# Optimization experiments

Measured on AMD Instinct MI355X. Metric: run time of the kernel, lower is better.

## Reference

```python
import jax, jax.numpy as jnp
import numpy as np


def setup_inputs() -> dict:
    key = jax.random.key(0)
    kx, kwl, kbl, kwr = jax.random.split(key, 4)
    B = 64          # batch of identical DAGs
    L = 11          # number of levels (leaves = level 0)
    NPL = 10000     # nodes per level
    K = 16          # children per non-leaf node
    N = L * NPL     # 110000 nodes per graph
    # Build a layered DAG: edges go child (level l-1) -> father (level l),
    # matching the module's convention edge_index[0]=child, edge_index[1]=father
    # (leaves are nodes with in-degree 0).
    rng = np.random.default_rng(0)
    srcs, dsts = [], []
    for l in range(1, L):
        fathers = np.arange(l * NPL, (l + 1) * NPL)
        children = rng.integers((l - 1) * NPL, l * NPL, size=(NPL, K))
        srcs.append(children.reshape(-1))
        dsts.append(np.repeat(fathers, K))
    edge_index = jnp.asarray(
        np.stack([np.concatenate(srcs), np.concatenate(dsts)]), dtype=jnp.int32
    )  # [2, E] with E = (L-1)*NPL*K = 1.6M
    x = jax.random.normal(kx, (B, N, 1), dtype=jnp.float32)
    w_l = jax.random.normal(kwl, (1, 1), dtype=jnp.float32)   # lin_l weight (1->1)
    b_l = jax.random.normal(kbl, (1,), dtype=jnp.float32) * 0.1  # lin_l bias
    w_r = jax.random.normal(kwr, (1, 1), dtype=jnp.float32)   # lin_r weight (no bias)
    return {"x": x, "w_l": w_l, "b_l": b_l, "w_r": w_r,
            "edge_index": edge_index, "num_levels": L - 1}


def _dagprop(x, w_l, b_l, w_r, edge_index, num_levels):
    # x: [B, N, 1] scalar node features for B identical DAGs.
    src, dst = edge_index[0], edge_index[1]
    N = x.shape[1]
    xb = x[..., 0]  # [B, N]
    indeg = jnp.zeros((N,), jnp.int32).at[dst].add(1)  # in-degree (children count)
    is_leaf = indeg == 0
    # Init: out[leaves] = tanh(x[leaves]); out[non-leaves] = lin_r(x) (no bias).
    out = jnp.where(is_leaf[None, :], jnp.tanh(xb), xb * w_r[0, 0])  # [B, N]
    visited = is_leaf
    inv_deg = 1.0 / jnp.maximum(indeg, 1).astype(xb.dtype)
    for _ in range(num_levels):
        # fathers whose children are ALL visited become the next frontier
        nvis = jnp.zeros((N,), jnp.int32).at[dst].add(visited[src].astype(jnp.int32))
        ready = (~visited) & (indeg > 0) & (nvis == indeg)
        # scatter-mean of children's outputs over all incoming edges (aggr='mean');
        # only consumed at 'ready' nodes, whose children are all visited.
        agg = jnp.zeros_like(out).at[:, dst].add(out[:, src]) * inv_deg[None, :]
        # out[next] = tanh(out[next] + lin_l(agg[next]))
        new = jnp.tanh(out + agg * w_l[0, 0] + b_l[0])
        out = jnp.where(ready[None, :], new, out)
        visited = visited | ready
    return out[..., None]  # [B, N, 1]


def reference(x, w_l, b_l, w_r, edge_index, num_levels):
    return _dagprop(x, w_l, b_l, w_r, edge_index, num_levels)
```

## Files before the change

### kernel.cpp

```cpp
#include <hip/hip_runtime.h>
#include <math.h>

#define BATCH  64
#define NPL    10000
#define NLEV   10
#define NNODE  110000
#define KCH    16
#define GSPLIT 8
#define FPB    (NPL / GSPLIT)
#define NPAIR  (BATCH / 2)
#define THREADS 1024
#define ITER    2

#define EXPITCH_F4 3072
#define EXPITCH_F  (EXPITCH_F4 * 4)
#define EXCH_FLOATS (2 * BATCH * EXPITCH_F)
#define FLAG_STRIDE 128

__device__ inline void coh_store(float* p, float v) {
    __hip_atomic_store(p, v, __ATOMIC_RELAXED, __HIP_MEMORY_SCOPE_AGENT);
}
__device__ inline void flag_set(unsigned char* p) {
    __hip_atomic_store(p, (unsigned char)1, __ATOMIC_RELAXED,
                       __HIP_MEMORY_SCOPE_AGENT);
}
__device__ inline unsigned long long flag_poll(const unsigned long long* p) {
    return __hip_atomic_load(p, __ATOMIC_RELAXED, __HIP_MEMORY_SCOPE_AGENT);
}

__device__ inline void coh_load4_x6(const float4* p0, const float4* p1,
                                    const float4* p2, const float4* p3,
                                    const float4* p4, const float4* p5,
                                    float4& a, float4& b, float4& c,
                                    float4& d, float4& e, float4& f) {
    asm volatile("global_load_dwordx4 %0, %6, off sc0 sc1\n\t"
                 "global_load_dwordx4 %1, %7, off sc0 sc1\n\t"
                 "global_load_dwordx4 %2, %8, off sc0 sc1\n\t"
                 "global_load_dwordx4 %3, %9, off sc0 sc1\n\t"
                 "global_load_dwordx4 %4, %10, off sc0 sc1\n\t"
                 "global_load_dwordx4 %5, %11, off sc0 sc1\n\t"
                 "s_waitcnt vmcnt(0)"
                 : "=&v"(a), "=&v"(b), "=&v"(c), "=&v"(d), "=&v"(e), "=&v"(f)
                 : "v"(p0), "v"(p1), "v"(p2), "v"(p3), "v"(p4), "v"(p5)
                 : "memory");
}

__global__ __launch_bounds__(THREADS, 4) void k_dag_pair(
    const float* __restrict__ x,
    float*       __restrict__ out,
    const int4*  __restrict__ src4,
    float*       __restrict__ exch,
    unsigned char* __restrict__ flags,
    const float* __restrict__ wl_p,
    const float* __restrict__ bl_p,
    const float* __restrict__ wr_p)
{
    __shared__ float bufA[EXPITCH_F];
    __shared__ float bufB[EXPITCH_F];
    const int blk  = blockIdx.x;
    const int pair = blk >> 3;
    const int q    = blk & 7;
    const int gA   = pair * 2, gB = gA + 1;
    const int tid  = threadIdx.x;
    const float wr   = wr_p[0];
    const float wl16 = wl_p[0] * (1.0f / 16.0f);
    const float bl   = bl_p[0];
    const float* __restrict__ xA = x   + (size_t)gA * NNODE;
    const float* __restrict__ xB = x   + (size_t)gB * NNODE;
    float*       __restrict__ oA = out + (size_t)gA * NNODE;
    float*       __restrict__ oB = out + (size_t)gB * NNODE;
    const int f0 = q * FPB;
    unsigned long long* flA = (unsigned long long*)(flags + gA * FLAG_STRIDE);
    unsigned long long* flB = (unsigned long long*)(flags + gB * FLAG_STRIDE);
    const unsigned long long ALL = 0x0101010101010101ULL;

    {
        float* exA0 = exch + (size_t)gA * EXPITCH_F;
        float* exB0 = exch + (size_t)gB * EXPITCH_F;
        for (int i = f0 + tid; i < f0 + FPB; i += THREADS) {
            float vA = tanhf(xA[i]); oA[i] = vA; coh_store(exA0 + i, vA);
            float vB = tanhf(xB[i]); oB[i] = vB; coh_store(exB0 + i, vB);
        }
    }
    __syncthreads();
    if (tid == 0) {
        flag_set((unsigned char*)flA + 0 * 8 + q);
        flag_set((unsigned char*)flB + 0 * 8 + q);
    }

    for (int l = 1; l <= NLEV; ++l) {
        const int pprev = (l - 1) & 1;
        if (tid == 0)
            while (flag_poll(flA + (l - 1)) != ALL) __builtin_amdgcn_s_sleep(1);
        if (tid == 256)
            while (flag_poll(flB + (l - 1)) != ALL) __builtin_amdgcn_s_sleep(1);
        asm volatile("" ::: "memory");
        __syncthreads();

        {
            const float4* eA = (const float4*)(exch +
                ((size_t)pprev * BATCH + gA) * EXPITCH_F);
            const float4* eB = (const float4*)(exch +
                ((size_t)pprev * BATCH + gB) * EXPITCH_F);
            float4 a0, a1, a2, b0, b1, b2;
            coh_load4_x6(eA + tid, eA + tid + 1024, eA + tid + 2048,
                         eB + tid, eB + tid + 1024, eB + tid + 2048,
                         a0, a1, a2, b0, b1, b2);
            float4* vA = (float4*)bufA;  float4* vB = (float4*)bufB;
            vA[tid] = a0; vA[tid + 1024] = a1; vA[tid + 2048] = a2;
            vB[tid] = b0; vB[tid + 1024] = b1; vB[tid + 2048] = b2;
        }
        __syncthreads();

        const int off   = (l - 1) * NPL;
        const int nodeb = l * NPL + f0;
        float* ewA = exch + ((size_t)(l & 1) * BATCH + gA) * EXPITCH_F + f0;
        float* ewB = exch + ((size_t)(l & 1) * BATCH + gB) * EXPITCH_F + f0;
        const int4* sp = src4 + (size_t)((l - 1) * NPL + f0) * (KCH / 4);
#pragma unroll
        for (int it = 0; it < ITER; ++it) {
            const int f = tid + it * THREADS;
            if (f < FPB) {
                const int4 c0 = sp[f * 4 + 0];
                const int4 c1 = sp[f * 4 + 1];
                const int4 c2 = sp[f * 4 + 2];
                const int4 c3 = sp[f * 4 + 3];
                float sA = bufA[c0.x - off] + bufA[c0.y - off]
                         + bufA[c0.z - off] + bufA[c0.w - off]
                         + bufA[c1.x - off] + bufA[c1.y - off]
                         + bufA[c1.z - off] + bufA[c1.w - off]
                         + bufA[c2.x - off] + bufA[c2.y - off]
                         + bufA[c2.z - off] + bufA[c2.w - off]
                         + bufA[c3.x - off] + bufA[c3.y - off]
                         + bufA[c3.z - off] + bufA[c3.w - off];
                float sB = bufB[c0.x - off] + bufB[c0.y - off]
                         + bufB[c0.z - off] + bufB[c0.w - off]
                         + bufB[c1.x - off] + bufB[c1.y - off]
                         + bufB[c1.z - off] + bufB[c1.w - off]
                         + bufB[c2.x - off] + bufB[c2.y - off]
                         + bufB[c2.z - off] + bufB[c2.w - off]
                         + bufB[c3.x - off] + bufB[c3.y - off]
                         + bufB[c3.z - off] + bufB[c3.w - off];
                const float vA = tanhf(fmaf(sA, wl16, fmaf(xA[nodeb + f], wr, bl)));
                const float vB = tanhf(fmaf(sB, wl16, fmaf(xB[nodeb + f], wr, bl)));
                oA[nodeb + f] = vA;
                oB[nodeb + f] = vB;
                if (l < NLEV) { coh_store(ewA + f, vA); coh_store(ewB + f, vB); }
            }
        }
        if (l < NLEV) {
            __syncthreads();
            if (tid == 0) {
                flag_set((unsigned char*)flA + l * 8 + q);
                flag_set((unsigned char*)flB + l * 8 + q);
            }
        }
    }
}

extern "C" void kernel_launch(void* const* d_in, const int* in_sizes, int n_in,
                              void* d_out, int out_size, void* d_ws, size_t ws_size,
                              hipStream_t stream) {
    const float* x  = (const float*)d_in[0];
    const float* wl = (const float*)d_in[1];
    const float* bl = (const float*)d_in[2];
    const float* wr = (const float*)d_in[3];
    const int*   ei = (const int*)d_in[4];

    const int4* src4 = (const int4*)ei;
    float* out  = (float*)d_out;
    float* exch = (float*)d_ws;
    unsigned char* flags = (unsigned char*)d_ws + (size_t)EXCH_FLOATS * sizeof(float);

    hipMemsetAsync(flags, 0, BATCH * FLAG_STRIDE, stream);
    k_dag_pair<<<NPAIR * GSPLIT, THREADS, 0, stream>>>(
        x, out, src4, exch, flags, wl, bl, wr);
}
```

Before: 153.6 us.

## Pipeline per-level exchange loads and publish graph A before graph B

Child indices and x values for each level are now prefetched before spinning on the readiness flags, so their latency hides behind the wait. The exchange loads for both graphs are issued together, but only graph A's data is awaited first. Graph A's gather and tanh run while graph B's loads are still in flight, and A's level flag is published before B is processed, so dependent blocks can start earlier. In exchange, every thread now polls the flags instead of one thread per graph, and correctness depends on hand-placed waitcnt and barrier ordering for the coherent stores.

```diff
diff --git a/kernel.cpp b/kernel.cpp
--- a/kernel.cpp
+++ b/kernel.cpp
@@ -10,7 +10,6 @@
 #define FPB    (NPL / GSPLIT)
 #define NPAIR  (BATCH / 2)
 #define THREADS 1024
-#define ITER    2
 
 #define EXPITCH_F4 3072
 #define EXPITCH_F  (EXPITCH_F4 * 4)
@@ -28,24 +27,41 @@
     return __hip_atomic_load(p, __ATOMIC_RELAXED, __HIP_MEMORY_SCOPE_AGENT);
 }
 
-__device__ inline void coh_load4_x6(const float4* p0, const float4* p1,
-                                    const float4* p2, const float4* p3,
-                                    const float4* p4, const float4* p5,
-                                    float4& a, float4& b, float4& c,
-                                    float4& d, float4& e, float4& f) {
-    asm volatile("global_load_dwordx4 %0, %6, off sc0 sc1\n\t"
-                 "global_load_dwordx4 %1, %7, off sc0 sc1\n\t"
-                 "global_load_dwordx4 %2, %8, off sc0 sc1\n\t"
-                 "global_load_dwordx4 %3, %9, off sc0 sc1\n\t"
-                 "global_load_dwordx4 %4, %10, off sc0 sc1\n\t"
-                 "global_load_dwordx4 %5, %11, off sc0 sc1\n\t"
-                 "s_waitcnt vmcnt(0)"
-                 : "=&v"(a), "=&v"(b), "=&v"(c), "=&v"(d), "=&v"(e), "=&v"(f)
-                 : "v"(p0), "v"(p1), "v"(p2), "v"(p3), "v"(p4), "v"(p5)
-                 : "memory");
+__device__ inline void coh_issue6_waitA(
+    const float4* pa0, const float4* pa1, const float4* pa2,
+    const float4* pb0, const float4* pb1, const float4* pb2,
+    float4& a0, float4& a1, float4& a2,
+    float4& b0, float4& b1, float4& b2) {
+    asm volatile(
+        "global_load_dwordx4 %0, %6, off sc0 sc1\n\t"
+        "global_load_dwordx4 %1, %7, off sc0 sc1\n\t"
+        "global_load_dwordx4 %2, %8, off sc0 sc1\n\t"
+        "global_load_dwordx4 %3, %9, off sc0 sc1\n\t"
+        "global_load_dwordx4 %4, %10, off sc0 sc1\n\t"
+        "global_load_dwordx4 %5, %11, off sc0 sc1\n\t"
+        "s_waitcnt vmcnt(3)"
+        : "=&v"(a0), "=&v"(a1), "=&v"(a2), "=&v"(b0), "=&v"(b1), "=&v"(b2)
+        : "v"(pa0), "v"(pa1), "v"(pa2), "v"(pb0), "v"(pb1), "v"(pb2)
+        : "memory");
+}
+__device__ inline void vm_wait0() {
+    asm volatile("s_waitcnt vmcnt(0)" ::: "memory");
+    __builtin_amdgcn_sched_barrier(0);
+}
+__device__ inline void barrier_lds() {
+    asm volatile("s_waitcnt lgkmcnt(0)" ::: "memory");
+    __builtin_amdgcn_sched_barrier(0);
+    __builtin_amdgcn_s_barrier();
+    __builtin_amdgcn_sched_barrier(0);
 }
 
-__global__ __launch_bounds__(THREADS, 4) void k_dag_pair(
+#define GATHER16(BUF, c0, c1, c2, c3, off)                                  \
+    (BUF[c0.x - off] + BUF[c0.y - off] + BUF[c0.z - off] + BUF[c0.w - off]  \
+   + BUF[c1.x - off] + BUF[c1.y - off] + BUF[c1.z - off] + BUF[c1.w - off]  \
+   + BUF[c2.x - off] + BUF[c2.y - off] + BUF[c2.z - off] + BUF[c2.w - off]  \
+   + BUF[c3.x - off] + BUF[c3.y - off] + BUF[c3.z - off] + BUF[c3.w - off])
+
+__global__ __launch_bounds__(THREADS, 4) void k_dag_pipe(
     const float* __restrict__ x,
     float*       __restrict__ out,
     const int4*  __restrict__ src4,
@@ -84,77 +100,75 @@
     }
     __syncthreads();
     if (tid == 0) {
-        flag_set((unsigned char*)flA + 0 * 8 + q);
-        flag_set((unsigned char*)flB + 0 * 8 + q);
+        flag_set((unsigned char*)flA + q);
+        flag_set((unsigned char*)flB + q);
     }
 
     for (int l = 1; l <= NLEV; ++l) {
         const int pprev = (l - 1) & 1;
-        if (tid == 0)
-            while (flag_poll(flA + (l - 1)) != ALL) __builtin_amdgcn_s_sleep(1);
-        if (tid == 256)
-            while (flag_poll(flB + (l - 1)) != ALL) __builtin_amdgcn_s_sleep(1);
+        const int off   = (l - 1) * NPL;
+        const int nodeb = l * NPL + f0;
+
+        const int4* sp = src4 + (size_t)((l - 1) * NPL + f0) * (KCH / 4);
+        const int4 p0 = sp[tid * 4 + 0];
+        const int4 p1 = sp[tid * 4 + 1];
+        const int4 p2 = sp[tid * 4 + 2];
+        const int4 p3 = sp[tid * 4 + 3];
+        const float xaf = xA[nodeb + tid];
+        const float xbf = xB[nodeb + tid];
+
+        while (flag_poll(flA + (l - 1)) != ALL) __builtin_amdgcn_s_sleep(1);
+        while (flag_poll(flB + (l - 1)) != ALL) __builtin_amdgcn_s_sleep(1);
         asm volatile("" ::: "memory");
-        __syncthreads();
 
-        {
-            const float4* eA = (const float4*)(exch +
-                ((size_t)pprev * BATCH + gA) * EXPITCH_F);
-            const float4* eB = (const float4*)(exch +
-                ((size_t)pprev * BATCH + gB) * EXPITCH_F);
-            float4 a0, a1, a2, b0, b1, b2;
-            coh_load4_x6(eA + tid, eA + tid + 1024, eA + tid + 2048,
+        const float4* eA = (const float4*)(exch + ((size_t)pprev * BATCH + gA) * EXPITCH_F);
+        const float4* eB = (const float4*)(exch + ((size_t)pprev * BATCH + gB) * EXPITCH_F);
+        float4 a0, a1, a2, b0, b1, b2;
+        coh_issue6_waitA(eA + tid, eA + tid + 1024, eA + tid + 2048,
                          eB + tid, eB + tid + 1024, eB + tid + 2048,
                          a0, a1, a2, b0, b1, b2);
-            float4* vA = (float4*)bufA;  float4* vB = (float4*)bufB;
-            vA[tid] = a0; vA[tid + 1024] = a1; vA[tid + 2048] = a2;
-            vB[tid] = b0; vB[tid + 1024] = b1; vB[tid + 2048] = b2;
+        { float4* v = (float4*)bufA; v[tid] = a0; v[tid+1024] = a1; v[tid+2048] = a2; }
+        barrier_lds();
+
+        float* ewA = exch + ((size_t)(l & 1) * BATCH + gA) * EXPITCH_F + f0;
+        {
+            float s = GATHER16(bufA, p0, p1, p2, p3, off);
+            float v = tanhf(fmaf(s, wl16, fmaf(xaf, wr, bl)));
+            oA[nodeb + tid] = v;
+            if (l < NLEV) coh_store(ewA + tid, v);
         }
+        if (tid + THREADS < FPB) {
+            const int f = tid + THREADS;
+            const int4 c0 = sp[f*4+0], c1 = sp[f*4+1], c2 = sp[f*4+2], c3 = sp[f*4+3];
+            float s = GATHER16(bufA, c0, c1, c2, c3, off);
+            float v = tanhf(fmaf(s, wl16, fmaf(xA[nodeb + f], wr, bl)));
+            oA[nodeb + f] = v;
+            if (l < NLEV) coh_store(ewA + f, v);
+        }
+
+        vm_wait0();
+        { float4* v = (float4*)bufB; v[tid] = b0; v[tid+1024] = b1; v[tid+2048] = b2; }
+        barrier_lds();
+        if (l < NLEV && tid == 0) flag_set((unsigned char*)flA + l * 8 + q);
+
+        float* ewB = exch + ((size_t)(l & 1) * BATCH + gB) * EXPITCH_F + f0;
+        {
+            float s = GATHER16(bufB, p0, p1, p2, p3, off);
+            float v = tanhf(fmaf(s, wl16, fmaf(xbf, wr, bl)));
+            oB[nodeb + tid] = v;
+            if (l < NLEV) coh_store(ewB + tid, v);
+        }
+        if (tid + THREADS < FPB) {
+            const int f = tid + THREADS;
+            const int4 c0 = sp[f*4+0], c1 = sp[f*4+1], c2 = sp[f*4+2], c3 = sp[f*4+3];
+            float s = GATHER16(bufB, c0, c1, c2, c3, off);
+            float v = tanhf(fmaf(s, wl16, fmaf(xB[nodeb + f], wr, bl)));
+            oB[nodeb + f] = v;
+            if (l < NLEV) coh_store(ewB + f, v);
+        }
+
         __syncthreads();
-
-        const int off   = (l - 1) * NPL;
-        const int nodeb = l * NPL + f0;
-        float* ewA = exch + ((size_t)(l & 1) * BATCH + gA) * EXPITCH_F + f0;
-        float* ewB = exch + ((size_t)(l & 1) * BATCH + gB) * EXPITCH_F + f0;
-        const int4* sp = src4 + (size_t)((l - 1) * NPL + f0) * (KCH / 4);
-#pragma unroll
-        for (int it = 0; it < ITER; ++it) {
-            const int f = tid + it * THREADS;
-            if (f < FPB) {
-                const int4 c0 = sp[f * 4 + 0];
-                const int4 c1 = sp[f * 4 + 1];
-                const int4 c2 = sp[f * 4 + 2];
-                const int4 c3 = sp[f * 4 + 3];
-                float sA = bufA[c0.x - off] + bufA[c0.y - off]
-                         + bufA[c0.z - off] + bufA[c0.w - off]
-                         + bufA[c1.x - off] + bufA[c1.y - off]
-                         + bufA[c1.z - off] + bufA[c1.w - off]
-                         + bufA[c2.x - off] + bufA[c2.y - off]
-                         + bufA[c2.z - off] + bufA[c2.w - off]
-                         + bufA[c3.x - off] + bufA[c3.y - off]
-                         + bufA[c3.z - off] + bufA[c3.w - off];
-                float sB = bufB[c0.x - off] + bufB[c0.y - off]
-                         + bufB[c0.z - off] + bufB[c0.w - off]
-                         + bufB[c1.x - off] + bufB[c1.y - off]
-                         + bufB[c1.z - off] + bufB[c1.w - off]
-                         + bufB[c2.x - off] + bufB[c2.y - off]
-                         + bufB[c2.z - off] + bufB[c2.w - off]
-                         + bufB[c3.x - off] + bufB[c3.y - off]
-                         + bufB[c3.z - off] + bufB[c3.w - off];
-                const float vA = tanhf(fmaf(sA, wl16, fmaf(xA[nodeb + f], wr, bl)));
-                const float vB = tanhf(fmaf(sB, wl16, fmaf(xB[nodeb + f], wr, bl)));
-                oA[nodeb + f] = vA;
-                oB[nodeb + f] = vB;
-                if (l < NLEV) { coh_store(ewA + f, vA); coh_store(ewB + f, vB); }
-            }
-        }
-        if (l < NLEV) {
-            __syncthreads();
-            if (tid == 0) {
-                flag_set((unsigned char*)flA + l * 8 + q);
-                flag_set((unsigned char*)flB + l * 8 + q);
-            }
-        }
+        if (l < NLEV && tid == 0) flag_set((unsigned char*)flB + l * 8 + q);
     }
 }
 
@@ -172,7 +186,7 @@
     float* exch = (float*)d_ws;
     unsigned char* flags = (unsigned char*)d_ws + (size_t)EXCH_FLOATS * sizeof(float);
 
-    hipMemsetAsync(flags, 0, BATCH * FLAG_STRIDE, stream);
-    k_dag_pair<<<NPAIR * GSPLIT, THREADS, 0, stream>>>(
+    (void)hipMemsetAsync(flags, 0, BATCH * FLAG_STRIDE, stream);
+    k_dag_pipe<<<NPAIR * GSPLIT, THREADS, 0, stream>>>(
         x, out, src4, exch, flags, wl, bl, wr);
 }
```

Result: slower. 156.9 us (+2.2%).
